# Kernel optimization log

Hardware: AMD Instinct MI355X
Metric: run time of the kernel (lower is better)

## Reference

```python
import jax, jax.numpy as jnp
import numpy as np

B, S, D, H = 2, 2048, 1024, 16
HD = D // H  # head size = 64

def setup_inputs() -> dict:
    key = jax.random.key(0)
    ks = jax.random.split(key, 12)
    sc = 0.02
    return {
        "hidden_states": jax.random.normal(ks[0], (B, S, D), jnp.float32),
        "attention_mask": jnp.zeros((B, S), jnp.float32),  # additive mask (0 = attend)
        "position_bias": jax.random.normal(ks[1], (H, S, S), jnp.float32) * sc,
        "Wq": jax.random.normal(ks[2], (D, D), jnp.float32) * sc,
        "bq": jnp.zeros((D,), jnp.float32),
        "Wk": jax.random.normal(ks[3], (D, D), jnp.float32) * sc,
        "bk": jnp.zeros((D,), jnp.float32),
        "Wv": jax.random.normal(ks[4], (D, D), jnp.float32) * sc,
        "bv": jnp.zeros((D,), jnp.float32),
        "Wo": jax.random.normal(ks[5], (D, D), jnp.float32) * sc,
        "bo": jnp.zeros((D,), jnp.float32),
    }

def reference(hidden_states, attention_mask, position_bias, Wq, bq, Wk, bk, Wv, bv, Wo, bo):
    b, s, _ = hidden_states.shape
    def heads(x):
        # [B,S,D] -> [B,H,S,HD]
        return x.reshape(b, s, H, HD).transpose(0, 2, 1, 3)
    q = heads(hidden_states @ Wq + bq)
    k = heads(hidden_states @ Wk + bk)
    v = heads(hidden_states @ Wv + bv)
    scores = jnp.einsum("bhqd,bhkd->bhqk", q, k) / jnp.sqrt(jnp.float32(HD))
    scores = scores + position_bias[None]                 # [1,H,S,S]
    scores = scores + attention_mask[:, None, None, :]    # [B,1,1,S]
    probs = jax.nn.softmax(scores, axis=-1)
    # dropout is identity in eval mode
    ctx = jnp.einsum("bhqk,bhkd->bhqd", probs, v)
    ctx = ctx.transpose(0, 2, 1, 3).reshape(b, s, D)
    return ctx @ Wo + bo
```

## Files before the change

kernel.cpp:

```cpp
#include <hip/hip_runtime.h>
#include <hip/hip_bf16.h>

#define B_  2
#define S_  2048
#define D_  1024
#define H_  16
#define HD_ 64
#define M_  (B_ * S_)

typedef unsigned short u16;
typedef __attribute__((ext_vector_type(8))) short short8;
typedef __attribute__((ext_vector_type(4))) float f32x4;

#define MFMA16(a, b, c) __builtin_amdgcn_mfma_f32_16x16x32_bf16(a, b, c, 0, 0, 0)

__device__ __forceinline__ u16 f2bf(float f) {
    union { float f; unsigned u; } v; v.f = f;
    unsigned r = v.u + 0x7FFFu + ((v.u >> 16) & 1u);
    return (u16)(r >> 16);
}

__device__ __forceinline__ void gl_lds16(const void* g, void* lds) {
    __builtin_amdgcn_global_load_lds(
        (const __attribute__((address_space(1))) unsigned int*)g,
        (__attribute__((address_space(3))) unsigned int*)lds, 16, 0, 0);
}

__global__ __launch_bounds__(256) void cvt_bf16(const float* __restrict__ x,
                                                u16* __restrict__ y) {
    const int i = (blockIdx.x * 256 + threadIdx.x) * 4;
    const float4 v = *(const float4*)(x + i);
    ushort4 o;
    o.x = f2bf(v.x); o.y = f2bf(v.y); o.z = f2bf(v.z); o.w = f2bf(v.w);
    *(ushort4*)(y + i) = o;
}

__global__ __launch_bounds__(256) void wt_trans(
    const float* __restrict__ w0, const float* __restrict__ w1,
    const float* __restrict__ w2, const float* __restrict__ w3,
    u16* __restrict__ t0, u16* __restrict__ t1,
    u16* __restrict__ t2, u16* __restrict__ t3) {
    const float* W; u16* T;
    switch (blockIdx.z) {
        case 0: W = w0; T = t0; break;
        case 1: W = w1; T = t1; break;
        case 2: W = w2; T = t2; break;
        default: W = w3; T = t3; break;
    }
    __shared__ float t[32][33];
    const int tid = threadIdx.x;
    const int kt = blockIdx.x, nt = blockIdx.y;
    const int r = tid >> 3, c4 = (tid & 7) * 4;
    const float4 v = *(const float4*)&W[(size_t)(kt * 32 + r) * D_ + nt * 32 + c4];
    t[c4 + 0][r] = v.x; t[c4 + 1][r] = v.y; t[c4 + 2][r] = v.z; t[c4 + 3][r] = v.w;
    __syncthreads();
    ushort4 o;
    o.x = f2bf(t[r][c4 + 0]); o.y = f2bf(t[r][c4 + 1]);
    o.z = f2bf(t[r][c4 + 2]); o.w = f2bf(t[r][c4 + 3]);
    *(ushort4*)&T[(size_t)(nt * 32 + r) * D_ + kt * 32 + c4] = o;
}

__global__ __launch_bounds__(256) void gemm_bt_bf16(
    const u16* __restrict__ A,
    const u16* __restrict__ Bt0, const u16* __restrict__ Bt1, const u16* __restrict__ Bt2,
    const float* __restrict__ bi0, const float* __restrict__ bi1, const float* __restrict__ bi2,
    void* __restrict__ o0, void* __restrict__ o1, void* __restrict__ o2,
    int mode) {
    const u16* Bt; const float* bias; void* outp;
    switch (blockIdx.z) {
        case 0: Bt = Bt0; bias = bi0; outp = o0; break;
        case 1: Bt = Bt1; bias = bi1; outp = o1; break;
        default: Bt = Bt2; bias = bi2; outp = o2; break;
    }
    __shared__ __align__(16) char smem[16384];

    const int tid = threadIdx.x;
    const int wave = tid >> 6, lane = tid & 63;
    const int quad = lane >> 4, l15 = lane & 15;
    const int wm = wave >> 1, wn = wave & 1;
    const int bm = blockIdx.x * 128, bn = blockIdx.y * 128;

    f32x4 acc[4][4];
#pragma unroll
    for (int i = 0; i < 4; ++i)
#pragma unroll
        for (int j = 0; j < 4; ++j) acc[i][j] = (f32x4)0.f;

    for (int k0 = 0; k0 < D_; k0 += 32) {
        __syncthreads();
#pragma unroll
        for (int i = 0; i < 2; ++i) {
            const int c = (wave * 2 + i) * 64 + lane;
            const int row = c >> 2, e = c & 3;
            gl_lds16(A  + (size_t)(bm + row) * D_ + k0 + e * 8,
                     smem + (wave * 2 + i) * 1024);
            gl_lds16(Bt + (size_t)(bn + row) * D_ + k0 + e * 8,
                     smem + 8192 + (wave * 2 + i) * 1024);
        }
        __syncthreads();

        short8 aF[4], bF[4];
#pragma unroll
        for (int mt = 0; mt < 4; ++mt)
            aF[mt] = *(const short8*)(smem + ((wm * 64 + mt * 16 + l15) * 32 + quad * 8) * 2);
#pragma unroll
        for (int nt = 0; nt < 4; ++nt)
            bF[nt] = *(const short8*)(smem + 8192 + ((wn * 64 + nt * 16 + l15) * 32 + quad * 8) * 2);
#pragma unroll
        for (int mt = 0; mt < 4; ++mt)
#pragma unroll
            for (int nt = 0; nt < 4; ++nt)
                acc[mt][nt] = MFMA16(aF[mt], bF[nt], acc[mt][nt]);
    }

    float bv[4];
#pragma unroll
    for (int nt = 0; nt < 4; ++nt) bv[nt] = bias[bn + wn * 64 + nt * 16 + l15];

    if (mode == 1) {
        u16* ob = (u16*)outp;
#pragma unroll
        for (int mt = 0; mt < 4; ++mt)
#pragma unroll
            for (int nt = 0; nt < 4; ++nt)
#pragma unroll
                for (int r = 0; r < 4; ++r) {
                    const int m = bm + wm * 64 + mt * 16 + quad * 4 + r;
                    const int n = bn + wn * 64 + nt * 16 + l15;
                    const int bb = m >> 11, ss = m & (S_ - 1);
                    const int hh = n >> 6,  dd = n & (HD_ - 1);
                    ob[(((size_t)bb * H_ + hh) * S_ + ss) * HD_ + dd] =
                        f2bf(acc[mt][nt][r] + bv[nt]);
                }
    } else {
        float* of = (float*)outp;
#pragma unroll
        for (int mt = 0; mt < 4; ++mt)
#pragma unroll
            for (int nt = 0; nt < 4; ++nt)
#pragma unroll
                for (int r = 0; r < 4; ++r) {
                    const int m = bm + wm * 64 + mt * 16 + quad * 4 + r;
                    const int n = bn + wn * 64 + nt * 16 + l15;
                    of[(size_t)m * D_ + n] = acc[mt][nt][r] + bv[nt];
                }
    }
}

#define QS_OFF 0
#define KS_OFF 16384
#define VT_OFF 24576
#define PS_OFF 33792
#define VT_LD 72
#define PS_LD 72

__global__ __launch_bounds__(256) void attn_mfma(
    const u16* __restrict__ Qg, const u16* __restrict__ Kg, const u16* __restrict__ Vg,
    const float* __restrict__ pb, const float* __restrict__ mask,
    u16* __restrict__ Cb) {
    __shared__ __align__(16) char smem[52224];
    u16* Vt = (u16*)(smem + VT_OFF);
    u16* Ps = (u16*)(smem + PS_OFF);

    const int tid = threadIdx.x;
    const int wave = tid >> 6, lane = tid & 63;
    const int quad = lane >> 4, l15 = lane & 15;

    const int b = blockIdx.x & 1, qblk = blockIdx.x >> 1;
    const int h = blockIdx.y;
    const int q0 = qblk * 128;

    const size_t bh = (size_t)b * H_ + h;
    const u16* Qb = Qg + bh * (S_ * HD_);
    const u16* Kb = Kg + bh * (S_ * HD_);
    const u16* Vb = Vg + bh * (S_ * HD_);

#pragma unroll
    for (int i = 0; i < 4; ++i) {
        const int c = (wave * 4 + i) * 64 + lane;
        const int q = c >> 3, e = c & 7, dc = e ^ (q & 7);
        gl_lds16(Qb + (size_t)(q0 + q) * HD_ + dc * 8,
                 smem + QS_OFF + (wave * 4 + i) * 1024);
    }

    f32x4 O[2][4];
    float mst[2][4], lst[2][4];
#pragma unroll
    for (int t2 = 0; t2 < 2; ++t2) {
#pragma unroll
        for (int nt = 0; nt < 4; ++nt) O[t2][nt] = (f32x4)0.f;
#pragma unroll
        for (int r = 0; r < 4; ++r) { mst[t2][r] = -1e30f; lst[t2][r] = 0.f; }
    }

    for (int kt = 0; kt < S_ / 64; ++kt) {
        const int k0 = kt * 64;
        __syncthreads();

#pragma unroll
        for (int i = 0; i < 2; ++i) {
            const int c = (wave * 2 + i) * 64 + lane;
            const int q = c >> 3, e = c & 7, dc = e ^ (q & 7);
            gl_lds16(Kb + (size_t)(k0 + q) * HD_ + dc * 8,
                     smem + KS_OFF + (wave * 2 + i) * 1024);
        }
        {
            const int k = tid & 63, dh = tid >> 6;
#pragma unroll
            for (int p = 0; p < 2; ++p) {
                const int d0 = dh * 16 + p * 8;
                u16 tmp[8];
                *(uint4*)tmp = *(const uint4*)(Vb + (size_t)(k0 + k) * HD_ + d0);
#pragma unroll
                for (int j = 0; j < 8; ++j) Vt[(d0 + j) * VT_LD + k] = tmp[j];
            }
        }
        float mk[4], pbv[2][4][4];
#pragma unroll
        for (int nt = 0; nt < 4; ++nt) mk[nt] = mask[b * S_ + k0 + nt * 16 + l15];
#pragma unroll
        for (int t2 = 0; t2 < 2; ++t2)
#pragma unroll
            for (int r = 0; r < 4; ++r) {
                const int qg = q0 + wave * 32 + t2 * 16 + quad * 4 + r;
                const float* rowp = pb + ((size_t)h * S_ + qg) * S_ + k0;
#pragma unroll
                for (int nt = 0; nt < 4; ++nt) pbv[t2][r][nt] = rowp[nt * 16 + l15];
            }
        __syncthreads();

        f32x4 sc[2][4];
#pragma unroll
        for (int t2 = 0; t2 < 2; ++t2)
#pragma unroll
            for (int nt = 0; nt < 4; ++nt) sc[t2][nt] = (f32x4)0.f;

        short8 aQ[2][2];
#pragma unroll
        for (int t2 = 0; t2 < 2; ++t2)
#pragma unroll
            for (int kc = 0; kc < 2; ++kc) {
                const int q = wave * 32 + t2 * 16 + l15;
                const int dc = kc * 4 + quad;
                aQ[t2][kc] = *(const short8*)(smem + QS_OFF + (q * 8 + (dc ^ (q & 7))) * 16);
            }
#pragma unroll
        for (int nt = 0; nt < 4; ++nt)
#pragma unroll
            for (int kc = 0; kc < 2; ++kc) {
                const int kk = nt * 16 + l15;
                const int dc = kc * 4 + quad;
                const short8 bK = *(const short8*)(smem + KS_OFF + (kk * 8 + (dc ^ (kk & 7))) * 16);
                sc[0][nt] = MFMA16(aQ[0][kc], bK, sc[0][nt]);
                sc[1][nt] = MFMA16(aQ[1][kc], bK, sc[1][nt]);
            }

#pragma unroll
        for (int t2 = 0; t2 < 2; ++t2)
#pragma unroll
            for (int r = 0; r < 4; ++r) {
                float s0 = fmaf(sc[t2][0][r], 0.125f, pbv[t2][r][0] + mk[0]);
                float s1 = fmaf(sc[t2][1][r], 0.125f, pbv[t2][r][1] + mk[1]);
                float s2 = fmaf(sc[t2][2][r], 0.125f, pbv[t2][r][2] + mk[2]);
                float s3 = fmaf(sc[t2][3][r], 0.125f, pbv[t2][r][3] + mk[3]);
                float rmax = fmaxf(fmaxf(s0, s1), fmaxf(s2, s3));
#pragma unroll
                for (int off = 1; off < 16; off <<= 1)
                    rmax = fmaxf(rmax, __shfl_xor(rmax, off, 64));
                const float mo = mst[t2][r];
                const float mn = fmaxf(mo, rmax);
                const float al = __expf(mo - mn);
                const float p0 = __expf(s0 - mn), p1 = __expf(s1 - mn);
                const float p2 = __expf(s2 - mn), p3 = __expf(s3 - mn);
                float ls = (p0 + p1) + (p2 + p3);
#pragma unroll
                for (int off = 1; off < 16; off <<= 1)
                    ls += __shfl_xor(ls, off, 64);
                mst[t2][r] = mn;
                lst[t2][r] = fmaf(lst[t2][r], al, ls);
                const int qr = wave * 32 + t2 * 16 + quad * 4 + r;
                Ps[qr * PS_LD +  0 + l15] = f2bf(p0);
                Ps[qr * PS_LD + 16 + l15] = f2bf(p1);
                Ps[qr * PS_LD + 32 + l15] = f2bf(p2);
                Ps[qr * PS_LD + 48 + l15] = f2bf(p3);
                O[t2][0][r] *= al; O[t2][1][r] *= al;
                O[t2][2][r] *= al; O[t2][3][r] *= al;
            }

        short8 aP[2][2];
#pragma unroll
        for (int t2 = 0; t2 < 2; ++t2)
#pragma unroll
            for (int kc = 0; kc < 2; ++kc) {
                const int q = wave * 32 + t2 * 16 + l15;
                aP[t2][kc] = *(const short8*)&Ps[q * PS_LD + kc * 32 + quad * 8];
            }
#pragma unroll
        for (int nt = 0; nt < 4; ++nt)
#pragma unroll
            for (int kc = 0; kc < 2; ++kc) {
                const int d = nt * 16 + l15;
                const short8 bV = *(const short8*)&Vt[d * VT_LD + kc * 32 + quad * 8];
                O[0][nt] = MFMA16(aP[0][kc], bV, O[0][nt]);
                O[1][nt] = MFMA16(aP[1][kc], bV, O[1][nt]);
            }
    }

#pragma unroll
    for (int t2 = 0; t2 < 2; ++t2)
#pragma unroll
        for (int r = 0; r < 4; ++r) {
            const float inv = 1.f / lst[t2][r];
            const int s = q0 + wave * 32 + t2 * 16 + quad * 4 + r;
            u16* dst = Cb + ((size_t)b * S_ + s) * D_ + h * HD_;
#pragma unroll
            for (int nt = 0; nt < 4; ++nt)
                dst[nt * 16 + l15] = f2bf(O[t2][nt][r] * inv);
        }
}

extern "C" void kernel_launch(void* const* d_in, const int* in_sizes, int n_in,
                              void* d_out, int out_size, void* d_ws, size_t ws_size,
                              hipStream_t stream) {
    const float* X    = (const float*)d_in[0];
    const float* mask = (const float*)d_in[1];
    const float* pb   = (const float*)d_in[2];
    const float* Wq   = (const float*)d_in[3];
    const float* bq   = (const float*)d_in[4];
    const float* Wk   = (const float*)d_in[5];
    const float* bk   = (const float*)d_in[6];
    const float* Wv   = (const float*)d_in[7];
    const float* bv   = (const float*)d_in[8];
    const float* Wo   = (const float*)d_in[9];
    const float* bo   = (const float*)d_in[10];
    float* out = (float*)d_out;

    u16* Xb  = (u16*)d_ws;
    u16* Wtq = Xb  + (size_t)M_ * D_;
    u16* Wtk = Wtq + (size_t)D_ * D_;
    u16* Wtv = Wtk + (size_t)D_ * D_;
    u16* Wto = Wtv + (size_t)D_ * D_;
    u16* Qw  = Wto + (size_t)D_ * D_;
    u16* Kw  = Qw  + (size_t)M_ * D_;
    u16* Vw  = Kw  + (size_t)M_ * D_;
    u16* Cb  = Vw  + (size_t)M_ * D_;

    cvt_bf16<<<(M_ * D_) / (256 * 4), 256, 0, stream>>>(X, Xb);
    wt_trans<<<dim3(32, 32, 4), 256, 0, stream>>>(Wq, Wk, Wv, Wo, Wtq, Wtk, Wtv, Wto);

    gemm_bt_bf16<<<dim3(M_ / 128, D_ / 128, 3), 256, 0, stream>>>(
        Xb, Wtq, Wtk, Wtv, bq, bk, bv, Qw, Kw, Vw, 1);

    attn_mfma<<<dim3((S_ / 128) * B_, H_), 256, 0, stream>>>(Qw, Kw, Vw, pb, mask, Cb);

    gemm_bt_bf16<<<dim3(M_ / 128, D_ / 128, 1), 256, 0, stream>>>(
        Cb, Wto, Wto, Wto, bo, bo, bo, out, out, out, 0);
}
```

Baseline: 529.3 us.

## Pre-transpose V globally, shrink attention tile to 64 queries, merge QKV GEMM grid

Adds a separate kernel that writes V transposed per head, so the attention kernel can load V^T tiles with async global-to-LDS copies instead of scattering a per-tile transpose through LDS. The attention block now covers 64 queries instead of 128, which cuts LDS use and registers so more blocks fit per CU (launch bounds set to 4). Q fragments are loaded once into registers outside the key loop. The QKV GEMM uses one contiguous weight buffer with a 2D grid, choosing bias and output by column block. In exchange there is an extra launch and a V round trip through memory, and each key/V tile is read by twice as many blocks.

```diff
diff --git a/kernel.cpp b/kernel.cpp
--- a/kernel.cpp
+++ b/kernel.cpp
@@ -60,18 +60,33 @@
     *(ushort4*)&T[(size_t)(nt * 32 + r) * D_ + kt * 32 + c4] = o;
 }
 
+__global__ __launch_bounds__(256) void v_trans(const u16* __restrict__ V,
+                                               u16* __restrict__ VT) {
+    __shared__ u16 t[64][72];
+    const int bh = blockIdx.x, s0 = blockIdx.y * 64;
+    const int tid = threadIdx.x;
+    const int ss = tid >> 2, cq = tid & 3;
+    const u16* src = V + ((size_t)bh * S_ + s0 + ss) * HD_ + cq * 16;
+    u16 buf[16];
+    *(uint4*)&buf[0] = *(const uint4*)&src[0];
+    *(uint4*)&buf[8] = *(const uint4*)&src[8];
+#pragma unroll
+    for (int j = 0; j < 16; ++j) t[cq * 16 + j][ss] = buf[j];
+    __syncthreads();
+    const int dd = tid >> 2;
+    u16 ob[16];
+#pragma unroll
+    for (int j = 0; j < 16; ++j) ob[j] = t[dd][cq * 16 + j];
+    u16* dst = VT + ((size_t)bh * HD_ + dd) * S_ + s0 + cq * 16;
+    *(uint4*)&dst[0] = *(uint4*)&ob[0];
+    *(uint4*)&dst[8] = *(uint4*)&ob[8];
+}
+
 __global__ __launch_bounds__(256) void gemm_bt_bf16(
-    const u16* __restrict__ A,
-    const u16* __restrict__ Bt0, const u16* __restrict__ Bt1, const u16* __restrict__ Bt2,
+    const u16* __restrict__ A, const u16* __restrict__ Bt,
     const float* __restrict__ bi0, const float* __restrict__ bi1, const float* __restrict__ bi2,
     void* __restrict__ o0, void* __restrict__ o1, void* __restrict__ o2,
     int mode) {
-    const u16* Bt; const float* bias; void* outp;
-    switch (blockIdx.z) {
-        case 0: Bt = Bt0; bias = bi0; outp = o0; break;
-        case 1: Bt = Bt1; bias = bi1; outp = o1; break;
-        default: Bt = Bt2; bias = bi2; outp = o2; break;
-    }
     __shared__ __align__(16) char smem[16384];
 
     const int tid = threadIdx.x;
@@ -79,6 +94,10 @@
     const int quad = lane >> 4, l15 = lane & 15;
     const int wm = wave >> 1, wn = wave & 1;
     const int bm = blockIdx.x * 128, bn = blockIdx.y * 128;
+
+    const int sel = bn >> 10;
+    const float* bias = (sel == 0) ? bi0 : (sel == 1) ? bi1 : bi2;
+    void* outp = (sel == 0) ? o0 : (sel == 1) ? o1 : o2;
 
     f32x4 acc[4][4];
 #pragma unroll
@@ -115,7 +134,8 @@
 
     float bv[4];
 #pragma unroll
-    for (int nt = 0; nt < 4; ++nt) bv[nt] = bias[bn + wn * 64 + nt * 16 + l15];
+    for (int nt = 0; nt < 4; ++nt)
+        bv[nt] = bias[(bn & 1023) + wn * 64 + nt * 16 + l15];
 
     if (mode == 1) {
         u16* ob = (u16*)outp;
@@ -126,7 +146,7 @@
 #pragma unroll
                 for (int r = 0; r < 4; ++r) {
                     const int m = bm + wm * 64 + mt * 16 + quad * 4 + r;
-                    const int n = bn + wn * 64 + nt * 16 + l15;
+                    const int n = (bn & 1023) + wn * 64 + nt * 16 + l15;
                     const int bb = m >> 11, ss = m & (S_ - 1);
                     const int hh = n >> 6,  dd = n & (HD_ - 1);
                     ob[(((size_t)bb * H_ + hh) * S_ + ss) * HD_ + dd] =
@@ -147,20 +167,18 @@
     }
 }
 
-#define QS_OFF 0
-#define KS_OFF 16384
-#define VT_OFF 24576
-#define PS_OFF 33792
-#define VT_LD 72
+#define AQ_OFF  0
+#define AK_OFF  8192
+#define AV_OFF  16384
+#define APS_OFF 24576
 #define PS_LD 72
 
-__global__ __launch_bounds__(256) void attn_mfma(
-    const u16* __restrict__ Qg, const u16* __restrict__ Kg, const u16* __restrict__ Vg,
+__global__ __launch_bounds__(256, 4) void attn_mfma(
+    const u16* __restrict__ Qg, const u16* __restrict__ Kg, const u16* __restrict__ VTg,
     const float* __restrict__ pb, const float* __restrict__ mask,
     u16* __restrict__ Cb) {
-    __shared__ __align__(16) char smem[52224];
-    u16* Vt = (u16*)(smem + VT_OFF);
-    u16* Ps = (u16*)(smem + PS_OFF);
+    __shared__ __align__(16) char smem[33792];
+    u16* Ps = (u16*)(smem + APS_OFF);
 
     const int tid = threadIdx.x;
     const int wave = tid >> 6, lane = tid & 63;
@@ -168,30 +186,36 @@
 
     const int b = blockIdx.x & 1, qblk = blockIdx.x >> 1;
     const int h = blockIdx.y;
-    const int q0 = qblk * 128;
+    const int q0 = qblk * 64;
 
     const size_t bh = (size_t)b * H_ + h;
-    const u16* Qb = Qg + bh * (S_ * HD_);
-    const u16* Kb = Kg + bh * (S_ * HD_);
-    const u16* Vb = Vg + bh * (S_ * HD_);
-
-#pragma unroll
-    for (int i = 0; i < 4; ++i) {
-        const int c = (wave * 4 + i) * 64 + lane;
+    const u16* Qb  = Qg  + bh * (S_ * HD_);
+    const u16* Kb  = Kg  + bh * (S_ * HD_);
+    const u16* VTb = VTg + bh * (HD_ * S_);
+
+#pragma unroll
+    for (int i = 0; i < 2; ++i) {
+        const int c = (wave * 2 + i) * 64 + lane;
         const int q = c >> 3, e = c & 7, dc = e ^ (q & 7);
         gl_lds16(Qb + (size_t)(q0 + q) * HD_ + dc * 8,
-                 smem + QS_OFF + (wave * 4 + i) * 1024);
-    }
-
-    f32x4 O[2][4];
-    float mst[2][4], lst[2][4];
-#pragma unroll
-    for (int t2 = 0; t2 < 2; ++t2) {
-#pragma unroll
-        for (int nt = 0; nt < 4; ++nt) O[t2][nt] = (f32x4)0.f;
-#pragma unroll
-        for (int r = 0; r < 4; ++r) { mst[t2][r] = -1e30f; lst[t2][r] = 0.f; }
-    }
+                 smem + AQ_OFF + (wave * 2 + i) * 1024);
+    }
+    __syncthreads();
+
+    short8 aQ[2];
+#pragma unroll
+    for (int kc = 0; kc < 2; ++kc) {
+        const int q = wave * 16 + l15;
+        const int dc = kc * 4 + quad;
+        aQ[kc] = *(const short8*)(smem + AQ_OFF + (q * 8 + (dc ^ (q & 7))) * 16);
+    }
+
+    f32x4 O[4];
+    float mst[4], lst[4];
+#pragma unroll
+    for (int nt = 0; nt < 4; ++nt) O[nt] = (f32x4)0.f;
+#pragma unroll
+    for (int r = 0; r < 4; ++r) { mst[r] = -1e30f; lst[r] = 0.f; }
 
     for (int kt = 0; kt < S_ / 64; ++kt) {
         const int k0 = kt * 64;
@@ -202,121 +226,91 @@
             const int c = (wave * 2 + i) * 64 + lane;
             const int q = c >> 3, e = c & 7, dc = e ^ (q & 7);
             gl_lds16(Kb + (size_t)(k0 + q) * HD_ + dc * 8,
-                     smem + KS_OFF + (wave * 2 + i) * 1024);
-        }
-        {
-            const int k = tid & 63, dh = tid >> 6;
-#pragma unroll
-            for (int p = 0; p < 2; ++p) {
-                const int d0 = dh * 16 + p * 8;
-                u16 tmp[8];
-                *(uint4*)tmp = *(const uint4*)(Vb + (size_t)(k0 + k) * HD_ + d0);
-#pragma unroll
-                for (int j = 0; j < 8; ++j) Vt[(d0 + j) * VT_LD + k] = tmp[j];
-            }
-        }
-        float mk[4], pbv[2][4][4];
+                     smem + AK_OFF + (wave * 2 + i) * 1024);
+            gl_lds16(VTb + (size_t)q * S_ + k0 + dc * 8,
+                     smem + AV_OFF + (wave * 2 + i) * 1024);
+        }
+
+        float mk[4], pbv[4][4];
 #pragma unroll
         for (int nt = 0; nt < 4; ++nt) mk[nt] = mask[b * S_ + k0 + nt * 16 + l15];
 #pragma unroll
-        for (int t2 = 0; t2 < 2; ++t2)
-#pragma unroll
-            for (int r = 0; r < 4; ++r) {
-                const int qg = q0 + wave * 32 + t2 * 16 + quad * 4 + r;
-                const float* rowp = pb + ((size_t)h * S_ + qg) * S_ + k0;
-#pragma unroll
-                for (int nt = 0; nt < 4; ++nt) pbv[t2][r][nt] = rowp[nt * 16 + l15];
-            }
+        for (int r = 0; r < 4; ++r) {
+            const int qg = q0 + wave * 16 + quad * 4 + r;
+            const float* rowp = pb + ((size_t)h * S_ + qg) * S_ + k0;
+#pragma unroll
+            for (int nt = 0; nt < 4; ++nt) pbv[r][nt] = rowp[nt * 16 + l15];
+        }
         __syncthreads();
 
-        f32x4 sc[2][4];
-#pragma unroll
-        for (int t2 = 0; t2 < 2; ++t2)
-#pragma unroll
-            for (int nt = 0; nt < 4; ++nt) sc[t2][nt] = (f32x4)0.f;
-
-        short8 aQ[2][2];
-#pragma unroll
-        for (int t2 = 0; t2 < 2; ++t2)
-#pragma unroll
-            for (int kc = 0; kc < 2; ++kc) {
-                const int q = wave * 32 + t2 * 16 + l15;
-                const int dc = kc * 4 + quad;
-                aQ[t2][kc] = *(const short8*)(smem + QS_OFF + (q * 8 + (dc ^ (q & 7))) * 16);
-            }
+        f32x4 sc[4];
+#pragma unroll
+        for (int nt = 0; nt < 4; ++nt) sc[nt] = (f32x4)0.f;
 #pragma unroll
         for (int nt = 0; nt < 4; ++nt)
 #pragma unroll
             for (int kc = 0; kc < 2; ++kc) {
                 const int kk = nt * 16 + l15;
                 const int dc = kc * 4 + quad;
-                const short8 bK = *(const short8*)(smem + KS_OFF + (kk * 8 + (dc ^ (kk & 7))) * 16);
-                sc[0][nt] = MFMA16(aQ[0][kc], bK, sc[0][nt]);
-                sc[1][nt] = MFMA16(aQ[1][kc], bK, sc[1][nt]);
+                const short8 bK = *(const short8*)(smem + AK_OFF + (kk * 8 + (dc ^ (kk & 7))) * 16);
+                sc[nt] = MFMA16(aQ[kc], bK, sc[nt]);
             }
 
 #pragma unroll
-        for (int t2 = 0; t2 < 2; ++t2)
-#pragma unroll
-            for (int r = 0; r < 4; ++r) {
-                float s0 = fmaf(sc[t2][0][r], 0.125f, pbv[t2][r][0] + mk[0]);
-                float s1 = fmaf(sc[t2][1][r], 0.125f, pbv[t2][r][1] + mk[1]);
-                float s2 = fmaf(sc[t2][2][r], 0.125f, pbv[t2][r][2] + mk[2]);
-                float s3 = fmaf(sc[t2][3][r], 0.125f, pbv[t2][r][3] + mk[3]);
-                float rmax = fmaxf(fmaxf(s0, s1), fmaxf(s2, s3));
-#pragma unroll
-                for (int off = 1; off < 16; off <<= 1)
-                    rmax = fmaxf(rmax, __shfl_xor(rmax, off, 64));
-                const float mo = mst[t2][r];
-                const float mn = fmaxf(mo, rmax);
-                const float al = __expf(mo - mn);
-                const float p0 = __expf(s0 - mn), p1 = __expf(s1 - mn);
-                const float p2 = __expf(s2 - mn), p3 = __expf(s3 - mn);
-                float ls = (p0 + p1) + (p2 + p3);
-#pragma unroll
-                for (int off = 1; off < 16; off <<= 1)
-                    ls += __shfl_xor(ls, off, 64);
-                mst[t2][r] = mn;
-                lst[t2][r] = fmaf(lst[t2][r], al, ls);
-                const int qr = wave * 32 + t2 * 16 + quad * 4 + r;
-                Ps[qr * PS_LD +  0 + l15] = f2bf(p0);
-                Ps[qr * PS_LD + 16 + l15] = f2bf(p1);
-                Ps[qr * PS_LD + 32 + l15] = f2bf(p2);
-                Ps[qr * PS_LD + 48 + l15] = f2bf(p3);
-                O[t2][0][r] *= al; O[t2][1][r] *= al;
-                O[t2][2][r] *= al; O[t2][3][r] *= al;
-            }
-
-        short8 aP[2][2];
-#pragma unroll
-        for (int t2 = 0; t2 < 2; ++t2)
-#pragma unroll
-            for (int kc = 0; kc < 2; ++kc) {
-                const int q = wave * 32 + t2 * 16 + l15;
-                aP[t2][kc] = *(const short8*)&Ps[q * PS_LD + kc * 32 + quad * 8];
-            }
+        for (int r = 0; r < 4; ++r) {
+            float s0 = fmaf(sc[0][r], 0.125f, pbv[r][0] + mk[0]);
+            float s1 = fmaf(sc[1][r], 0.125f, pbv[r][1] + mk[1]);
+            float s2 = fmaf(sc[2][r], 0.125f, pbv[r][2] + mk[2]);
+            float s3 = fmaf(sc[3][r], 0.125f, pbv[r][3] + mk[3]);
+            float rmax = fmaxf(fmaxf(s0, s1), fmaxf(s2, s3));
+#pragma unroll
+            for (int off = 1; off < 16; off <<= 1)
+                rmax = fmaxf(rmax, __shfl_xor(rmax, off, 64));
+            const float mo = mst[r];
+            const float mn = fmaxf(mo, rmax);
+            const float al = __expf(mo - mn);
+            const float p0 = __expf(s0 - mn), p1 = __expf(s1 - mn);
+            const float p2 = __expf(s2 - mn), p3 = __expf(s3 - mn);
+            float ls = (p0 + p1) + (p2 + p3);
+#pragma unroll
+            for (int off = 1; off < 16; off <<= 1)
+                ls += __shfl_xor(ls, off, 64);
+            mst[r] = mn;
+            lst[r] = fmaf(lst[r], al, ls);
+            const int qr = wave * 16 + quad * 4 + r;
+            Ps[qr * PS_LD +  0 + l15] = f2bf(p0);
+            Ps[qr * PS_LD + 16 + l15] = f2bf(p1);
+            Ps[qr * PS_LD + 32 + l15] = f2bf(p2);
+            Ps[qr * PS_LD + 48 + l15] = f2bf(p3);
+            O[0][r] *= al; O[1][r] *= al; O[2][r] *= al; O[3][r] *= al;
+        }
+
+        short8 aP[2];
+#pragma unroll
+        for (int kc = 0; kc < 2; ++kc) {
+            const int q = wave * 16 + l15;
+            aP[kc] = *(const short8*)&Ps[q * PS_LD + kc * 32 + quad * 8];
+        }
 #pragma unroll
         for (int nt = 0; nt < 4; ++nt)
 #pragma unroll
             for (int kc = 0; kc < 2; ++kc) {
                 const int d = nt * 16 + l15;
-                const short8 bV = *(const short8*)&Vt[d * VT_LD + kc * 32 + quad * 8];
-                O[0][nt] = MFMA16(aP[0][kc], bV, O[0][nt]);
-                O[1][nt] = MFMA16(aP[1][kc], bV, O[1][nt]);
+                const int dc = kc * 4 + quad;
+                const short8 bV = *(const short8*)(smem + AV_OFF + (d * 8 + (dc ^ (d & 7))) * 16);
+                O[nt] = MFMA16(aP[kc], bV, O[nt]);
             }
     }
 
 #pragma unroll
-    for (int t2 = 0; t2 < 2; ++t2)
-#pragma unroll
-        for (int r = 0; r < 4; ++r) {
-            const float inv = 1.f / lst[t2][r];
-            const int s = q0 + wave * 32 + t2 * 16 + quad * 4 + r;
-            u16* dst = Cb + ((size_t)b * S_ + s) * D_ + h * HD_;
-#pragma unroll
-            for (int nt = 0; nt < 4; ++nt)
-                dst[nt * 16 + l15] = f2bf(O[t2][nt][r] * inv);
-        }
+    for (int r = 0; r < 4; ++r) {
+        const float inv = 1.f / lst[r];
+        const int s = q0 + wave * 16 + quad * 4 + r;
+        u16* dst = Cb + ((size_t)b * S_ + s) * D_ + h * HD_;
+#pragma unroll
+        for (int nt = 0; nt < 4; ++nt)
+            dst[nt * 16 + l15] = f2bf(O[nt][r] * inv);
+    }
 }
 
 extern "C" void kernel_launch(void* const* d_in, const int* in_sizes, int n_in,
@@ -335,24 +329,26 @@
     const float* bo   = (const float*)d_in[10];
     float* out = (float*)d_out;
 
-    u16* Xb  = (u16*)d_ws;
-    u16* Wtq = Xb  + (size_t)M_ * D_;
-    u16* Wtk = Wtq + (size_t)D_ * D_;
-    u16* Wtv = Wtk + (size_t)D_ * D_;
-    u16* Wto = Wtv + (size_t)D_ * D_;
-    u16* Qw  = Wto + (size_t)D_ * D_;
-    u16* Kw  = Qw  + (size_t)M_ * D_;
-    u16* Vw  = Kw  + (size_t)M_ * D_;
-    u16* Cb  = Vw  + (size_t)M_ * D_;
+    u16* Xb    = (u16*)d_ws;
+    u16* WtQKV = Xb    + (size_t)M_ * D_;
+    u16* Wto   = WtQKV + (size_t)3 * D_ * D_;
+    u16* Qw    = Wto   + (size_t)D_ * D_;
+    u16* Kw    = Qw    + (size_t)M_ * D_;
+    u16* Vw    = Kw    + (size_t)M_ * D_;
+    u16* Cb    = Vw    + (size_t)M_ * D_;
+    u16* VTw   = Cb    + (size_t)M_ * D_;
 
     cvt_bf16<<<(M_ * D_) / (256 * 4), 256, 0, stream>>>(X, Xb);
-    wt_trans<<<dim3(32, 32, 4), 256, 0, stream>>>(Wq, Wk, Wv, Wo, Wtq, Wtk, Wtv, Wto);
-
-    gemm_bt_bf16<<<dim3(M_ / 128, D_ / 128, 3), 256, 0, stream>>>(
-        Xb, Wtq, Wtk, Wtv, bq, bk, bv, Qw, Kw, Vw, 1);
-
-    attn_mfma<<<dim3((S_ / 128) * B_, H_), 256, 0, stream>>>(Qw, Kw, Vw, pb, mask, Cb);
-
-    gemm_bt_bf16<<<dim3(M_ / 128, D_ / 128, 1), 256, 0, stream>>>(
-        Cb, Wto, Wto, Wto, bo, bo, bo, out, out, out, 0);
-}
+    wt_trans<<<dim3(32, 32, 4), 256, 0, stream>>>(
+        Wq, Wk, Wv, Wo, WtQKV, WtQKV + (size_t)D_ * D_, WtQKV + (size_t)2 * D_ * D_, Wto);
+
+    gemm_bt_bf16<<<dim3(M_ / 128, 3 * D_ / 128), 256, 0, stream>>>(
+        Xb, WtQKV, bq, bk, bv, Qw, Kw, Vw, 1);
+
+    v_trans<<<dim3(B_ * H_, S_ / 64), 256, 0, stream>>>(Vw, VTw);
+
+    attn_mfma<<<dim3((S_ / 64) * B_, H_), 256, 0, stream>>>(Qw, Kw, VTw, pb, mask, Cb);
+
+    gemm_bt_bf16<<<dim3(M_ / 128, D_ / 128), 256, 0, stream>>>(
+        Cb, Wto, bo, bo, bo, out, out, out, 0);
+}
```

Result: faster. 513.6 us (-3.0%).
